# Performance work log

Measured on AMD Instinct MI355X. Metric: run time of the kernel, lower is better.

Reference implementation:

```python
import jax, jax.numpy as jnp
import numpy as np
import math

# static config
NH, HD, HID = 16, 128, 2048
ROT = 64            # head_dim * partial_rotary_factor(0.5)
EPS = 1e-6
GROUPS = 8
CHUNK = 64
THETA = 10000.0
LAYER_IDX, N_LAYERS = 1, 32
B, S = 2, 2048


def _base_slopes(n):
    # power-of-two branch of HF ALiBi slopes
    start = 2 ** (-(2 ** (-(math.log2(n) - 3))))
    return [start * (start ** i) for i in range(n)]

# per-head log-decay (negative): slope = -base * (1 - (l-1)/(L-1) + 1e-5)
SLOPE = jnp.asarray(
    -np.array(_base_slopes(NH), dtype=np.float32)
    * (1.0 - (LAYER_IDX - 1) / (N_LAYERS - 1) + 1e-5),
    dtype=jnp.float32)  # [NH]


def _rmsnorm(x, w):
    return x * jax.lax.rsqrt(jnp.mean(x * x, axis=-1, keepdims=True) + EPS) * w


def _partial_rope(x, positions):
    # x: [B,S,NH,HD]; neox-style rotary on first ROT dims, rest passthrough
    half = ROT // 2
    inv_freq = 1.0 / (THETA ** (jnp.arange(half, dtype=jnp.float32) / half))
    ang = positions.astype(jnp.float32)[:, None] * inv_freq       # [S, half]
    cos = jnp.cos(ang)[None, :, None, :]
    sin = jnp.sin(ang)[None, :, None, :]
    x1, x2, rest = x[..., :half], x[..., half:ROT], x[..., ROT:]
    return jnp.concatenate(
        [x1 * cos - x2 * sin, x2 * cos + x1 * sin, rest], axis=-1)


def setup_inputs() -> dict:
    key = jax.random.key(0)
    ks = jax.random.split(key, 4)
    return {
        'positions': jnp.arange(S, dtype=jnp.int32),
        'hidden_states': jax.random.normal(ks[0], (B, S, HID), jnp.float32),
        'recurrent_state': jnp.zeros((B, NH, HD, HD), jnp.float32),
        'w_qkv': jax.random.normal(ks[1], (HID, 3 * NH * HD), jnp.float32) * 0.02,
        'w_g': jax.random.normal(ks[2], (HID, NH * HD), jnp.float32) * 0.02,
        'w_dense': jax.random.normal(ks[3], (NH * HD, HID), jnp.float32) * 0.02,
        'q_norm_w': jnp.ones((HD,), jnp.float32),
        'k_norm_w': jnp.ones((HD,), jnp.float32),
        'g_norm_w': jnp.ones((NH * HD,), jnp.float32),
    }


def reference(positions, hidden_states, recurrent_state, w_qkv, w_g, w_dense,
              q_norm_w, k_norm_w, g_norm_w):
    # fused QKV projection
    qkv = hidden_states @ w_qkv                       # [B,S,3*NH*HD]
    q, k, v = jnp.split(qkv, 3, axis=-1)
    q = q.reshape(B, S, NH, HD)
    k = k.reshape(B, S, NH, HD)
    v = v.reshape(B, S, NH, HD)

    # QK RMSNorm then partial rotary
    q = _partial_rope(_rmsnorm(q, q_norm_w), positions)
    k = _partial_rope(_rmsnorm(k, k_norm_w), positions)

    # chunked ALiBi-decayed linear attention:
    #   S_t = lam * S_{t-1} + k_t v_t^T ; o_t = q_t S_t, lam = exp(slope)
    NC = S // CHUNK
    qc = q.reshape(B, NC, CHUNK, NH, HD).transpose(1, 0, 3, 2, 4)  # [NC,B,NH,C,HD]
    kc = k.reshape(B, NC, CHUNK, NH, HD).transpose(1, 0, 3, 2, 4)
    vc = v.reshape(B, NC, CHUNK, NH, HD).transpose(1, 0, 3, 2, 4)

    t = jnp.arange(CHUNK, dtype=jnp.float32)
    # intra-chunk causal decay mask lam^(i-j), i>=j: [NH,C,C]
    dec_mask = jnp.where(t[:, None] >= t[None, :],
                         jnp.exp(SLOPE[:, None, None] * (t[:, None] - t[None, :])),
                         0.0)
    q_dec = jnp.exp(SLOPE[:, None] * (t[None, :] + 1.0))            # [NH,C] lam^(i+1)
    k_dec = jnp.exp(SLOPE[:, None] * (CHUNK - 1.0 - t[None, :]))    # [NH,C] lam^(C-1-j)
    lam_C = jnp.exp(SLOPE * CHUNK)                                   # [NH]

    def step(state, inp):
        qb, kb, vb = inp                                  # [B,NH,C,HD]
        scores = jnp.einsum('bhid,bhjd->bhij', qb, kb) * dec_mask[None]
        o_intra = jnp.einsum('bhij,bhjd->bhid', scores, vb)
        o_inter = jnp.einsum('bhid,bhde->bhie', qb * q_dec[None, :, :, None], state)
        new_state = (state * lam_C[None, :, None, None]
                     + jnp.einsum('bhjd,bhje->bhde', kb * k_dec[None, :, :, None], vb))
        return new_state, o_intra + o_inter

    _, o = jax.lax.scan(step, recurrent_state, (qc, kc, vc))  # o: [NC,B,NH,C,HD]
    o = o.transpose(1, 0, 3, 2, 4).reshape(B, S, NH * HD)

    # GroupRMSNorm on attention output, sigmoid gate, output projection
    og = o.reshape(B, S, GROUPS, (NH * HD) // GROUPS)
    og = og * jax.lax.rsqrt(jnp.mean(og * og, axis=-1, keepdims=True) + EPS)
    o = og.reshape(B, S, NH * HD) * g_norm_w
    o = o * jax.nn.sigmoid(hidden_states @ w_g)
    return o @ w_dense
```

## Files before the change

### kernel.cpp

```cpp
#include <hip/hip_runtime.h>
#include <hip/hip_bf16.h>
#include <math.h>

#define NH   16
#define HD   128
#define HID  2048
#define NKV  6144
#define B_   2
#define S_   2048
#define NC   32
#define CHUNK_ 64
#define GROUPS_ 8

typedef __bf16 bf16_t;
typedef bf16_t bf16x8 __attribute__((ext_vector_type(8)));
typedef float  f32x4  __attribute__((ext_vector_type(4)));

__device__ __forceinline__ float b2f(unsigned int u) {
    union { unsigned int u; float f; } c; c.u = (u & 0xffffu) << 16; return c.f;
}
__device__ __forceinline__ unsigned int f2b(float f) {
    union { float f; unsigned int u; } c; c.f = f;
    unsigned int u = c.u;
    return (u + 0x7fffu + ((u >> 16) & 1u)) >> 16;
}

#define GLOAD_LDS16(gp, lp) __builtin_amdgcn_global_load_lds(                     \
    (const __attribute__((address_space(1))) void*)(gp),                          \
    (__attribute__((address_space(3))) void*)(lp), 16, 0, 0)

__global__ __launch_bounds__(256) void cvt_bf16(const float* __restrict__ in,
                                                unsigned short* __restrict__ out, int n8)
{
    int i = blockIdx.x * 256 + threadIdx.x;
    if (i >= n8) return;
    const float4* p = (const float4*)in + (size_t)i * 2;
    float4 a = p[0], b = p[1];
    uint4 o;
    o.x = f2b(a.x) | (f2b(a.y) << 16);
    o.y = f2b(a.z) | (f2b(a.w) << 16);
    o.z = f2b(b.x) | (f2b(b.y) << 16);
    o.w = f2b(b.z) | (f2b(b.w) << 16);
    ((uint4*)out)[i] = o;
}

__global__ __launch_bounds__(256) void transpose_cvt(const float* __restrict__ in,
                                                     unsigned short* __restrict__ out,
                                                     int Kdim, int Ndim)
{
    __shared__ float tile[32][33];
    int ntx = Ndim >> 5;
    int bx = blockIdx.x % ntx;
    int by = blockIdx.x / ntx;
    int lx = threadIdx.x & 31, ly = threadIdx.x >> 5;
    int r0 = by * 32, c0 = bx * 32;
    #pragma unroll
    for (int r = 0; r < 4; ++r)
        tile[ly + r * 8][lx] = in[(size_t)(r0 + ly + r * 8) * Ndim + c0 + lx];
    __syncthreads();
    #pragma unroll
    for (int r = 0; r < 4; ++r)
        out[(size_t)(c0 + ly + r * 8) * Kdim + r0 + lx] = (unsigned short)f2b(tile[lx][ly + r * 8]);
}


__device__ __forceinline__ void ld_fr4(bf16x8 (&d)[4][2], const bf16_t* b, int s0, int ri) {
    #pragma unroll
    for (int i = 0; i < 4; ++i)
        #pragma unroll
        for (int k = 0; k < 2; ++k)
            d[i][k] = *(const bf16x8*)(b + (((s0 + i) * 2 + k) << 9) + ri);
}
__device__ __forceinline__ void ld_fr2(bf16x8 (&d)[2][2], const bf16_t* b, int s0, int ri) {
    #pragma unroll
    for (int i = 0; i < 2; ++i)
        #pragma unroll
        for (int k = 0; k < 2; ++k)
            d[i][k] = *(const bf16x8*)(b + (((s0 + i) * 2 + k) << 9) + ri);
}
__device__ __forceinline__ void mfma_quad(f32x4 (&a)[4][2], const bf16x8 (&af)[4][2],
                                          const bf16x8 (&bv)[2][2]) {
    #pragma unroll
    for (int mt = 0; mt < 4; ++mt)
        #pragma unroll
        for (int nt = 0; nt < 2; ++nt)
            #pragma unroll
            for (int ks = 0; ks < 2; ++ks)
                a[mt][nt] = __builtin_amdgcn_mfma_f32_16x16x32_bf16(af[mt][ks], bv[nt][ks], a[mt][nt], 0, 0, 0);
}

#define BAR()     asm volatile("s_barrier" ::: "memory")
#define VMCNT0()  asm volatile("s_waitcnt vmcnt(0)" ::: "memory")

__global__ __launch_bounds__(512, 2) void gemm_qg_256(const bf16_t* __restrict__ A,
                                                      const bf16_t* __restrict__ Bt,
                                                      unsigned short* __restrict__ Cq,
                                                      unsigned short* __restrict__ Cg)
{
    __shared__ bf16_t Asm[2][2][8192];
    __shared__ bf16_t Bsm[2][2][8192];
    const int K  = HID;
    const int NT = K / 64;

    int tid  = threadIdx.x;
    int wave = tid >> 6, lane = tid & 63;
    int wm = wave >> 2, wn = wave & 3;
    int l16 = lane & 15, quad = lane >> 4;
    int wm4 = wm * 4, wn2 = wn * 2;

    int bid = blockIdx.x;
    int xcd = bid & 7, idx = bid >> 3;
    int by  = (xcd >> 2) * 8 + (idx >> 3);
    int bx  = (xcd & 3) * 8 + (idx & 7);

    int rd_in = ((l16 << 5) | (quad << 3)) ^ (((l16 >> 3) & 1) << 4);

    int ch = lane ^ ((lane & 32) >> 4);
    int rr = ch >> 2;
    int cc = (ch & 3) * 8;

    const bf16_t* aSrc0 = A  + (size_t)(by * 256 +       wave * 16 + rr) * K + cc;
    const bf16_t* aSrc1 = A  + (size_t)(by * 256 + 128 + wave * 16 + rr) * K + cc;
    const bf16_t* bSrc0 = Bt + (size_t)(bx * 256 +       wave * 16 + rr) * K + cc;
    const bf16_t* bSrc1 = Bt + (size_t)(bx * 256 + 128 + wave * 16 + rr) * K + cc;

#define STAGE_A(h, t) do {                                                        \
        const bf16_t* _g = ((h) ? aSrc1 : aSrc0) + (size_t)(t) * 64;              \
        bf16_t* _l = &Asm[(t) & 1][(h)][wave * 1024 + lane * 8];                  \
        GLOAD_LDS16(_g,      _l);                                                 \
        GLOAD_LDS16(_g + 32, _l + 512); } while (0)
#define STAGE_B(h, t) do {                                                        \
        const bf16_t* _g = ((h) ? bSrc1 : bSrc0) + (size_t)(t) * 64;              \
        bf16_t* _l = &Bsm[(t) & 1][(h)][wave * 1024 + lane * 8];                  \
        GLOAD_LDS16(_g,      _l);                                                 \
        GLOAD_LDS16(_g + 32, _l + 512); } while (0)

    f32x4 acc[2][2][4][2];
    #pragma unroll
    for (int a0 = 0; a0 < 2; ++a0)
        #pragma unroll
        for (int a1 = 0; a1 < 2; ++a1)
            #pragma unroll
            for (int a2 = 0; a2 < 4; ++a2)
                #pragma unroll
                for (int a3 = 0; a3 < 2; ++a3) { f32x4 z = {0.f,0.f,0.f,0.f}; acc[a0][a1][a2][a3] = z; }

    STAGE_A(0, 0); STAGE_B(0, 0); STAGE_A(1, 0); STAGE_B(1, 0);
    VMCNT0();
    BAR();

    #pragma unroll 2
    for (int t = 0; t < NT - 1; ++t) {
        const int buf = t & 1;
        STAGE_A(0, t + 1); STAGE_B(0, t + 1); STAGE_A(1, t + 1); STAGE_B(1, t + 1);
        {
            bf16x8 afA[4][2], afB[4][2], bf0[2][2], bf1[2][2];
            ld_fr4(afA, &Asm[buf][0][0], wm4, rd_in);
            ld_fr2(bf0, &Bsm[buf][0][0], wn2, rd_in);
            mfma_quad(acc[0][0], afA, bf0);
            ld_fr2(bf1, &Bsm[buf][1][0], wn2, rd_in);
            mfma_quad(acc[0][1], afA, bf1);
            ld_fr4(afB, &Asm[buf][1][0], wm4, rd_in);
            mfma_quad(acc[1][1], afB, bf1);
            mfma_quad(acc[1][0], afB, bf0);
        }
        VMCNT0();
        BAR();
    }
    {
        const int buf = (NT - 1) & 1;
        bf16x8 afA[4][2], afB[4][2], bf0[2][2], bf1[2][2];
        ld_fr4(afA, &Asm[buf][0][0], wm4, rd_in);
        ld_fr2(bf0, &Bsm[buf][0][0], wn2, rd_in);
        mfma_quad(acc[0][0], afA, bf0);
        ld_fr2(bf1, &Bsm[buf][1][0], wn2, rd_in);
        mfma_quad(acc[0][1], afA, bf1);
        ld_fr4(afB, &Asm[buf][1][0], wm4, rd_in);
        mfma_quad(acc[1][1], afB, bf1);
        mfma_quad(acc[1][0], afB, bf0);
    }
#undef STAGE_A
#undef STAGE_B

    unsigned short* Cc; int Nn, colbase;
    if (bx < 24) { Cc = Cq; Nn = NKV; colbase = bx * 256; }
    else         { Cc = Cg; Nn = HID; colbase = bx * 256 - NKV; }
    int row0 = by * 256 + wm * 64 + quad * 4;
    int col0 = colbase + wn * 32 + l16;
    #pragma unroll
    for (int mh = 0; mh < 2; ++mh)
        #pragma unroll
        for (int nh = 0; nh < 2; ++nh)
            #pragma unroll
            for (int mt = 0; mt < 4; ++mt)
                #pragma unroll
                for (int nt = 0; nt < 2; ++nt) {
                    int col = col0 + nh * 128 + nt * 16;
                    #pragma unroll
                    for (int r = 0; r < 4; ++r) {
                        int row = row0 + mh * 128 + mt * 16 + r;
                        Cc[(size_t)row * Nn + col] = (unsigned short)f2b(acc[mh][nh][mt][nt][r]);
                    }
                }
}

__global__ __launch_bounds__(256, 2) void gemm_out_128(const bf16_t* __restrict__ A,
                                                       const bf16_t* __restrict__ Bt,
                                                       float* __restrict__ C)
{
    __shared__ bf16_t As[2][4096];
    __shared__ bf16_t Bs[2][4096];
    const int K  = HID;
    const int NT = K / 32;

    int tid  = threadIdx.x;
    int wave = tid >> 6, lane = tid & 63;
    int wm2 = wave >> 1, wn2 = wave & 1;
    int l16 = lane & 15, quad = lane >> 4;
    int w2 = wave * 2;

    int bid = blockIdx.x;
    int xcd = bid & 7, idx = bid >> 3;
    int by  = (xcd >> 1) * 8 + (idx >> 3);
    int bx  = (xcd & 1) * 8 + (idx & 7);

    int rd_in = ((l16 << 5) | (quad << 3)) ^ (((l16 >> 3) & 1) << 4);
    int ch = lane ^ ((lane & 32) >> 4);
    int rr = ch >> 2;
    int cc = (ch & 3) * 8;

    const bf16_t* aSrc = A  + (size_t)(by * 128 + w2 * 16 + rr) * K + cc;
    const bf16_t* bSrc = Bt + (size_t)(bx * 128 + w2 * 16 + rr) * K + cc;

#define OSTAGE(t) do {                                                            \
        const int nb_ = (t) & 1;                                                  \
        const bf16_t* _ga = aSrc + (size_t)(t) * 32;                              \
        const bf16_t* _gb = bSrc + (size_t)(t) * 32;                              \
        GLOAD_LDS16(_ga,                  &As[nb_][w2 * 512 + lane * 8]);         \
        GLOAD_LDS16(_ga + (size_t)16 * K, &As[nb_][w2 * 512 + 512 + lane * 8]);   \
        GLOAD_LDS16(_gb,                  &Bs[nb_][w2 * 512 + lane * 8]);         \
        GLOAD_LDS16(_gb + (size_t)16 * K, &Bs[nb_][w2 * 512 + 512 + lane * 8]); } while (0)

    f32x4 acc[4][4];
    #pragma unroll
    for (int i = 0; i < 4; ++i)
        #pragma unroll
        for (int j = 0; j < 4; ++j) { f32x4 z = {0.f,0.f,0.f,0.f}; acc[i][j] = z; }

#define OCOMP(t) do {                                                             \
        const int b_ = (t) & 1;                                                   \
        bf16x8 af_[4], bf_[4];                                                    \
        _Pragma("unroll")                                                         \
        for (int i = 0; i < 4; ++i)                                               \
            af_[i] = *(const bf16x8*)(&As[b_][((wm2 * 4 + i) << 9) + rd_in]);     \
        _Pragma("unroll")                                                         \
        for (int j = 0; j < 4; ++j)                                               \
            bf_[j] = *(const bf16x8*)(&Bs[b_][((wn2 * 4 + j) << 9) + rd_in]);     \
        _Pragma("unroll")                                                         \
        for (int i = 0; i < 4; ++i)                                               \
            _Pragma("unroll")                                                     \
            for (int j = 0; j < 4; ++j)                                           \
                acc[i][j] = __builtin_amdgcn_mfma_f32_16x16x32_bf16(af_[i], bf_[j], acc[i][j], 0, 0, 0); } while (0)

    OSTAGE(0);
    VMCNT0();
    BAR();
    #pragma unroll 2
    for (int t = 0; t < NT - 1; ++t) {
        OSTAGE(t + 1);
        OCOMP(t);
        VMCNT0();
        BAR();
    }
    OCOMP(NT - 1);
#undef OSTAGE
#undef OCOMP

    #pragma unroll
    for (int i = 0; i < 4; ++i)
        #pragma unroll
        for (int j = 0; j < 4; ++j) {
            int col = bx * 128 + wn2 * 64 + j * 16 + l16;
            #pragma unroll
            for (int r = 0; r < 4; ++r) {
                int row = by * 128 + wm2 * 64 + i * 16 + quad * 4 + r;
                C[(size_t)row * HID + col] = acc[i][j][r];
            }
        }
}

__global__ __launch_bounds__(256) void norm_rope(unsigned short* __restrict__ qkv,
                                                 const int* __restrict__ positions,
                                                 const float* __restrict__ qw,
                                                 const float* __restrict__ kw)
{
    int bs = blockIdx.x;
    int s  = bs & (S_ - 1);
    int tid = threadIdx.x;
    int l16 = tid & 15;
    unsigned short* base = qkv + (size_t)bs * NKV;
    float pos = (float)positions[s];

    #pragma unroll
    for (int p = 0; p < 2; ++p) {
        int rr = p * 16 + (tid >> 4);
        int qk = rr >> 4;
        int h  = rr & 15;
        unsigned short* row = base + qk * HID + h * HD;
        const float* w = qk ? kw : qw;
        uint4 v = *(const uint4*)(row + l16 * 8);
        float x[8];
        x[0] = b2f(v.x); x[1] = b2f(v.x >> 16);
        x[2] = b2f(v.y); x[3] = b2f(v.y >> 16);
        x[4] = b2f(v.z); x[5] = b2f(v.z >> 16);
        x[6] = b2f(v.w); x[7] = b2f(v.w >> 16);
        float ss = 0.f;
        #pragma unroll
        for (int t = 0; t < 8; ++t) ss += x[t] * x[t];
        ss += __shfl_xor(ss, 1); ss += __shfl_xor(ss, 2);
        ss += __shfl_xor(ss, 4); ss += __shfl_xor(ss, 8);
        float inv = rsqrtf(ss * (1.0f / 128.0f) + 1e-6f);
        float n[8];
        #pragma unroll
        for (int t = 0; t < 8; ++t) n[t] = x[t] * inv * w[l16 * 8 + t];
        float pr[8];
        #pragma unroll
        for (int t = 0; t < 8; ++t) pr[t] = __shfl_xor(n[t], 4);
        if (l16 < 8) {
            #pragma unroll
            for (int t = 0; t < 8; ++t) {
                int dim = l16 * 8 + t;
                int i = dim & 31;
                float ang = pos * exp2f(-(float)i * 0.4152410118609203f);
                float cs = cosf(ang), sn = sinf(ang);
                n[t] = (dim < 32) ? (n[t] * cs - pr[t] * sn) : (n[t] * cs + pr[t] * sn);
            }
        }
        uint4 o;
        o.x = f2b(n[0]) | (f2b(n[1]) << 16);
        o.y = f2b(n[2]) | (f2b(n[3]) << 16);
        o.z = f2b(n[4]) | (f2b(n[5]) << 16);
        o.w = f2b(n[6]) | (f2b(n[7]) << 16);
        *(uint4*)(row + l16 * 8) = o;
    }
}

__global__ __launch_bounds__(256) void chunk_kv(const unsigned short* __restrict__ qkv,
                                                unsigned short* __restrict__ wbuf)
{
    __shared__ unsigned short kt[128 * 72];
    __shared__ unsigned short vt[128 * 72];
    int bi = blockIdx.x;
    int c = bi & 31, bh = bi >> 5, h = bh & 15, b = bh >> 4;
    int tid = threadIdx.x;
    float slope = -exp2f(-0.5f * (float)(h + 1)) * (1.0f + 1e-5f);

    const unsigned short* kbase = qkv + ((size_t)(b * S_ + c * CHUNK_)) * NKV + HID + h * HD;
    const unsigned short* vbase = kbase + HID;

    for (int idx = tid; idx < 4096; idx += 256) {
        int j = idx >> 6, p = idx & 63;
        unsigned int ku = *(const unsigned int*)(kbase + (size_t)j * NKV + p * 2);
        kt[(2 * p) * 72 + j]     = (unsigned short)(ku & 0xffffu);
        kt[(2 * p + 1) * 72 + j] = (unsigned short)(ku >> 16);
        float kd = expf(slope * (float)(63 - j));
        unsigned int vu = *(const unsigned int*)(vbase + (size_t)j * NKV + p * 2);
        vt[(2 * p) * 72 + j]     = (unsigned short)f2b(b2f(vu) * kd);
        vt[(2 * p + 1) * 72 + j] = (unsigned short)f2b(b2f(vu >> 16) * kd);
    }
    __syncthreads();

    int lane = tid & 63, wave = tid >> 6;
    int wm = (wave >> 1) * 64;
    int wn = (wave & 1) * 64;
    int l16 = lane & 15, quad = lane >> 4;

    f32x4 acc[4][4];
    #pragma unroll
    for (int i = 0; i < 4; ++i)
        #pragma unroll
        for (int j = 0; j < 4; ++j) { f32x4 z = {0.f,0.f,0.f,0.f}; acc[i][j] = z; }

    #pragma unroll
    for (int ks = 0; ks < 64; ks += 32) {
        bf16x8 af[4], bf[4];
        #pragma unroll
        for (int t = 0; t < 4; ++t) {
            af[t] = *(const bf16x8*)((const bf16_t*)vt + (wm + t * 16 + l16) * 72 + ks + quad * 8);
            bf[t] = *(const bf16x8*)((const bf16_t*)kt + (wn + t * 16 + l16) * 72 + ks + quad * 8);
        }
        #pragma unroll
        for (int mt = 0; mt < 4; ++mt)
            #pragma unroll
            for (int nt = 0; nt < 4; ++nt)
                acc[mt][nt] = __builtin_amdgcn_mfma_f32_16x16x32_bf16(af[mt], bf[nt], acc[mt][nt], 0, 0, 0);
    }

    unsigned short* wp = wbuf + ((size_t)bi << 14);
    #pragma unroll
    for (int mt = 0; mt < 4; ++mt)
        #pragma unroll
        for (int nt = 0; nt < 4; ++nt) {
            int dcol = wn + nt * 16 + l16;
            #pragma unroll
            for (int r = 0; r < 4; ++r) {
                int erow = wm + mt * 16 + quad * 4 + r;
                wp[(size_t)erow * 128 + dcol] = (unsigned short)f2b(acc[mt][nt][r]);
            }
        }
}

__global__ __launch_bounds__(256) void state_scan(const unsigned short* __restrict__ wbuf,
                                                  const float* __restrict__ rs0,
                                                  unsigned short* __restrict__ stbuf)
{
    int bi = blockIdx.x;
    int es = bi & 15, bh = bi >> 4, h = bh & 15, b = bh >> 4;
    int tid = threadIdx.x;
    float slope = -exp2f(-0.5f * (float)(h + 1)) * (1.0f + 1e-5f);
    float lam = expf(slope * 64.0f);

    int e  = es * 8 + (tid >> 5);
    int d0 = (tid & 31) * 4;

    float S[4];
    const float* rp = rs0 + ((size_t)(b * NH + h)) * HD * HD + e;
    #pragma unroll
    for (int t = 0; t < 4; ++t) S[t] = rp[(size_t)(d0 + t) * HD];

    size_t off = (size_t)e * 128 + d0;
    size_t base = (((size_t)bh * NC) << 14) + off;
    uint2 w0 = *(const uint2*)(wbuf + base);
    uint2 w1 = *(const uint2*)(wbuf + base + (1 << 14));
    for (int c = 0; c < NC; ++c) {
        uint2 o;
        o.x = f2b(S[0]) | (f2b(S[1]) << 16);
        o.y = f2b(S[2]) | (f2b(S[3]) << 16);
        *(uint2*)(stbuf + base) = o;
        uint2 w2 = w1;
        if (c + 2 < NC) w2 = *(const uint2*)(wbuf + base + (2 << 14));
        S[0] = S[0] * lam + b2f(w0.x);
        S[1] = S[1] * lam + b2f(w0.x >> 16);
        S[2] = S[2] * lam + b2f(w0.y);
        S[3] = S[3] * lam + b2f(w0.y >> 16);
        w0 = w1; w1 = w2;
        base += (1 << 14);
    }
}

__global__ __launch_bounds__(256) void chunk_out(const unsigned short* __restrict__ qkv,
                                                 const unsigned short* __restrict__ stbuf,
                                                 unsigned short* __restrict__ obuf)
{
    __shared__ unsigned short qs[64 * 136];
    __shared__ unsigned short kss[64 * 136];
    __shared__ unsigned short vt[128 * 72];
    __shared__ unsigned short sc[64 * 72];

    int bi = blockIdx.x;
    int c = bi & 31, bh = bi >> 5, h = bh & 15, b = bh >> 4;
    int tid = threadIdx.x;
    float slope = -exp2f(-0.5f * (float)(h + 1)) * (1.0f + 1e-5f);

    int lane = tid & 63, wave = tid >> 6;
    int l16 = lane & 15, quad = lane >> 4;
    int wn3 = wave * 32;

    const unsigned short* stp = stbuf + (((size_t)bh * NC + c) << 14);
    bf16x8 bsf[4][2];
    #pragma unroll
    for (int ksp4 = 0; ksp4 < 4; ++ksp4)
        #pragma unroll
        for (int nt = 0; nt < 2; ++nt)
            bsf[ksp4][nt] = *(const bf16x8*)((const bf16_t*)stp +
                (size_t)(wn3 + nt * 16 + l16) * 128 + ksp4 * 32 + quad * 8);

    const unsigned short* qrow = qkv + ((size_t)(b * S_ + c * CHUNK_)) * NKV + h * HD;
    const unsigned short* krow = qrow + HID;
    for (int idx = tid; idx < 1024; idx += 256) {
        int row = idx >> 4, c8 = (idx & 15) * 8;
        *(uint4*)(qs  + row * 136 + c8) = *(const uint4*)(qrow + (size_t)row * NKV + c8);
        *(uint4*)(kss + row * 136 + c8) = *(const uint4*)(krow + (size_t)row * NKV + c8);
    }
    const unsigned short* vbase = qrow + 2 * HID;
    for (int idx = tid; idx < 4096; idx += 256) {
        int j = idx >> 6, p = idx & 63;
        unsigned int vu = *(const unsigned int*)(vbase + (size_t)j * NKV + p * 2);
        vt[(2 * p) * 72 + j]     = (unsigned short)(vu & 0xffffu);
        vt[(2 * p + 1) * 72 + j] = (unsigned short)(vu >> 16);
    }
    __syncthreads();

    {
        f32x4 accS[4];
        #pragma unroll
        for (int t = 0; t < 4; ++t) { f32x4 z = {0.f,0.f,0.f,0.f}; accS[t] = z; }
        #pragma unroll
        for (int ksp = 0; ksp < 128; ksp += 32) {
            bf16x8 aq = *(const bf16x8*)((const bf16_t*)qs + (wave * 16 + l16) * 136 + ksp + quad * 8);
            #pragma unroll
            for (int nt = 0; nt < 4; ++nt) {
                bf16x8 bk = *(const bf16x8*)((const bf16_t*)kss + (nt * 16 + l16) * 136 + ksp + quad * 8);
                accS[nt] = __builtin_amdgcn_mfma_f32_16x16x32_bf16(aq, bk, accS[nt], 0, 0, 0);
            }
        }
        float ad[4];
        #pragma unroll
        for (int r = 0; r < 4; ++r) ad[r] = expf(slope * (float)(wave * 16 + quad * 4 + r));
        #pragma unroll
        for (int nt = 0; nt < 4; ++nt) {
            int j = nt * 16 + l16;
            float bd = expf(-slope * (float)j);
            #pragma unroll
            for (int r = 0; r < 4; ++r) {
                int i = wave * 16 + quad * 4 + r;
                float v = (i >= j) ? accS[nt][r] * ad[r] * bd : 0.0f;
                sc[i * 72 + j] = (unsigned short)f2b(v);
            }
        }
    }
    __syncthreads();

    f32x4 accI[4][2], accE[4][2];
    #pragma unroll
    for (int i = 0; i < 4; ++i)
        #pragma unroll
        for (int j = 0; j < 2; ++j) { f32x4 z = {0.f,0.f,0.f,0.f}; accI[i][j] = z; accE[i][j] = z; }

    #pragma unroll
    for (int ksp = 0; ksp < 64; ksp += 32) {
        bf16x8 as[4], bv[2];
        #pragma unroll
        for (int mt = 0; mt < 4; ++mt)
            as[mt] = *(const bf16x8*)((const bf16_t*)sc + (mt * 16 + l16) * 72 + ksp + quad * 8);
        #pragma unroll
        for (int nt = 0; nt < 2; ++nt)
            bv[nt] = *(const bf16x8*)((const bf16_t*)vt + (wn3 + nt * 16 + l16) * 72 + ksp + quad * 8);
        #pragma unroll
        for (int mt = 0; mt < 4; ++mt)
            #pragma unroll
            for (int nt = 0; nt < 2; ++nt)
                accI[mt][nt] = __builtin_amdgcn_mfma_f32_16x16x32_bf16(as[mt], bv[nt], accI[mt][nt], 0, 0, 0);
    }
    #pragma unroll
    for (int ksp4 = 0; ksp4 < 4; ++ksp4) {
        bf16x8 aq[4];
        #pragma unroll
        for (int mt = 0; mt < 4; ++mt)
            aq[mt] = *(const bf16x8*)((const bf16_t*)qs + (mt * 16 + l16) * 136 + ksp4 * 32 + quad * 8);
        #pragma unroll
        for (int mt = 0; mt < 4; ++mt)
            #pragma unroll
            for (int nt = 0; nt < 2; ++nt)
                accE[mt][nt] = __builtin_amdgcn_mfma_f32_16x16x32_bf16(aq[mt], bsf[ksp4][nt], accE[mt][nt], 0, 0, 0);
    }

    #pragma unroll
    for (int mt = 0; mt < 4; ++mt) {
        #pragma unroll
        for (int r = 0; r < 4; ++r) {
            int i = mt * 16 + quad * 4 + r;
            float qd = expf(slope * (float)(i + 1));
            int orow = b * S_ + c * CHUNK_ + i;
            #pragma unroll
            for (int nt = 0; nt < 2; ++nt) {
                int col = h * HD + wn3 + nt * 16 + l16;
                float o = accI[mt][nt][r] + qd * accE[mt][nt][r];
                obuf[(size_t)orow * 2048 + col] = (unsigned short)f2b(o);
            }
        }
    }
}

__global__ __launch_bounds__(256) void gnorm_gate(const unsigned short* __restrict__ o,
                                                  unsigned short* __restrict__ gate,
                                                  const float* __restrict__ gw)
{
    int row = blockIdx.x >> 3;
    int g   = blockIdx.x & 7;
    int col = g * 256 + threadIdx.x;
    size_t idx = (size_t)row * 2048 + col;
    float ov = b2f(o[idx]);
    float ss = ov * ov;
    #pragma unroll
    for (int off = 32; off > 0; off >>= 1) ss += __shfl_xor(ss, off);
    __shared__ float part[4];
    if ((threadIdx.x & 63) == 0) part[threadIdx.x >> 6] = ss;
    __syncthreads();
    float tot = part[0] + part[1] + part[2] + part[3];
    float inv = rsqrtf(tot * (1.0f / 256.0f) + 1e-6f);
    float gv = b2f(gate[idx]);
    float sig = 1.0f / (1.0f + expf(-gv));
    gate[idx] = (unsigned short)f2b(ov * inv * gw[col] * sig);
}

extern "C" void kernel_launch(void* const* d_in, const int* in_sizes, int n_in,
                              void* d_out, int out_size, void* d_ws, size_t ws_size,
                              hipStream_t stream) {
    const int*   positions = (const int*)d_in[0];
    const float* hidden    = (const float*)d_in[1];
    const float* rstate    = (const float*)d_in[2];
    const float* w_qkv     = (const float*)d_in[3];
    const float* w_g       = (const float*)d_in[4];
    const float* w_dense   = (const float*)d_in[5];
    const float* q_norm_w  = (const float*)d_in[6];
    const float* k_norm_w  = (const float*)d_in[7];
    const float* g_norm_w  = (const float*)d_in[8];
    float* out = (float*)d_out;

    const int MR = B_ * S_;

    char* w = (char*)d_ws;
    unsigned short* qkv  = (unsigned short*)w;            w += (size_t)MR * NKV * 2;
    unsigned short* gbuf = (unsigned short*)w;            w += (size_t)MR * 2048 * 2;
    unsigned short* wdT  = (unsigned short*)w;            w += (size_t)HID * HID * 2;
    char* regionA = w;                                    w += (size_t)MR * HID * 2 + (size_t)8192 * HID * 2;
    char* regionB = w;
    unsigned short* hbf   = (unsigned short*)regionA;
    unsigned short* btQG  = (unsigned short*)(regionA + (size_t)MR * HID * 2);
    unsigned short* wqT   = btQG;
    unsigned short* wgT   = btQG + (size_t)NKV * HID;
    unsigned short* stbuf = (unsigned short*)regionA;
    unsigned short* wbuf  = (unsigned short*)regionB;
    unsigned short* obuf  = (unsigned short*)regionB;

    cvt_bf16<<<dim3((MR * HID / 8 + 255) / 256), dim3(256), 0, stream>>>(hidden, hbf, MR * HID / 8);
    transpose_cvt<<<dim3((HID / 32) * (NKV / 32)), dim3(256), 0, stream>>>(w_qkv, wqT, HID, NKV);
    transpose_cvt<<<dim3((HID / 32) * (HID / 32)), dim3(256), 0, stream>>>(w_g, wgT, HID, HID);
    transpose_cvt<<<dim3((HID / 32) * (HID / 32)), dim3(256), 0, stream>>>(w_dense, wdT, HID, HID);

    gemm_qg_256<<<dim3(512), dim3(512), 0, stream>>>(
        (const bf16_t*)hbf, (const bf16_t*)btQG, qkv, gbuf);
    norm_rope<<<dim3(B_ * S_), dim3(256), 0, stream>>>(qkv, positions, q_norm_w, k_norm_w);

    chunk_kv<<<dim3(B_ * NH * NC), dim3(256), 0, stream>>>(qkv, wbuf);
    state_scan<<<dim3(B_ * NH * 16), dim3(256), 0, stream>>>(wbuf, rstate, stbuf);
    chunk_out<<<dim3(B_ * NH * NC), dim3(256), 0, stream>>>(qkv, stbuf, obuf);

    gnorm_gate<<<dim3(MR * GROUPS_), dim3(256), 0, stream>>>(obuf, gbuf, g_norm_w);
    gemm_out_128<<<dim3(512), dim3(256), 0, stream>>>(
        (const bf16_t*)gbuf, (const bf16_t*)wdT, out);
}
```

Before: 424.1 us.

## Fuse norm/rope into chunk kernels, merge weight transposes, vectorize gate norm

Removes the standalone norm_rope kernel. Q/K RMSNorm and partial RoPE are now applied in shared memory inside chunk_kv and chunk_out, so qkv is no longer read and rewritten in a separate pass. The two QKV/G weight transposes are merged into one launch. The state buffer layout becomes MFMA-fragment-friendly so state_scan can use 16-byte loads with deeper prefetch and chunk_out can read state fragments contiguously. gnorm_gate is rewritten to process a full row per block with 8-wide vectors. The cost is that K normalization is recomputed in both chunk kernels, and the chunk kernels use more shared memory.

```diff
diff --git a/kernel.cpp b/kernel.cpp
--- a/kernel.cpp
+++ b/kernel.cpp
@@ -28,6 +28,9 @@
 #define GLOAD_LDS16(gp, lp) __builtin_amdgcn_global_load_lds(                     \
     (const __attribute__((address_space(1))) void*)(gp),                          \
     (__attribute__((address_space(3))) void*)(lp), 16, 0, 0)
+
+#define BAR()     asm volatile("s_barrier" ::: "memory")
+#define VMCNT0()  asm volatile("s_waitcnt vmcnt(0)" ::: "memory")
 
 __global__ __launch_bounds__(256) void cvt_bf16(const float* __restrict__ in,
                                                 unsigned short* __restrict__ out, int n8)
@@ -63,6 +66,26 @@
         out[(size_t)(c0 + ly + r * 8) * Kdim + r0 + lx] = (unsigned short)f2b(tile[lx][ly + r * 8]);
 }
 
+__global__ __launch_bounds__(256) void transpose_qg(const float* __restrict__ wq,
+                                                    const float* __restrict__ wg,
+                                                    unsigned short* __restrict__ out)
+{
+    __shared__ float tile[32][33];
+    int bx = blockIdx.x & 255;
+    int by = blockIdx.x >> 8;
+    int lx = threadIdx.x & 31, ly = threadIdx.x >> 5;
+    const float* in; int Ndim, c0;
+    if (bx < 192) { in = wq; Ndim = NKV; c0 = bx * 32; }
+    else          { in = wg; Ndim = HID; c0 = (bx - 192) * 32; }
+    int r0 = by * 32;
+    #pragma unroll
+    for (int r = 0; r < 4; ++r)
+        tile[ly + r * 8][lx] = in[(size_t)(r0 + ly + r * 8) * Ndim + c0 + lx];
+    __syncthreads();
+    #pragma unroll
+    for (int r = 0; r < 4; ++r)
+        out[(size_t)(bx * 32 + ly + r * 8) * HID + r0 + lx] = (unsigned short)f2b(tile[lx][ly + r * 8]);
+}
 
 __device__ __forceinline__ void ld_fr4(bf16x8 (&d)[4][2], const bf16_t* b, int s0, int ri) {
     #pragma unroll
@@ -88,9 +111,6 @@
             for (int ks = 0; ks < 2; ++ks)
                 a[mt][nt] = __builtin_amdgcn_mfma_f32_16x16x32_bf16(af[mt][ks], bv[nt][ks], a[mt][nt], 0, 0, 0);
 }
-
-#define BAR()     asm volatile("s_barrier" ::: "memory")
-#define VMCNT0()  asm volatile("s_waitcnt vmcnt(0)" ::: "memory")
 
 __global__ __launch_bounds__(512, 2) void gemm_qg_256(const bf16_t* __restrict__ A,
                                                       const bf16_t* __restrict__ Bt,
@@ -114,7 +134,6 @@
     int bx  = (xcd & 3) * 8 + (idx & 7);
 
     int rd_in = ((l16 << 5) | (quad << 3)) ^ (((l16 >> 3) & 1) << 4);
-
     int ch = lane ^ ((lane & 32) >> 4);
     int rr = ch >> 2;
     int cc = (ch & 3) * 8;
@@ -289,65 +308,51 @@
         }
 }
 
-__global__ __launch_bounds__(256) void norm_rope(unsigned short* __restrict__ qkv,
-                                                 const int* __restrict__ positions,
-                                                 const float* __restrict__ qw,
-                                                 const float* __restrict__ kw)
-{
-    int bs = blockIdx.x;
-    int s  = bs & (S_ - 1);
-    int tid = threadIdx.x;
-    int l16 = tid & 15;
-    unsigned short* base = qkv + (size_t)bs * NKV;
-    float pos = (float)positions[s];
-
-    #pragma unroll
-    for (int p = 0; p < 2; ++p) {
-        int rr = p * 16 + (tid >> 4);
-        int qk = rr >> 4;
-        int h  = rr & 15;
-        unsigned short* row = base + qk * HID + h * HD;
-        const float* w = qk ? kw : qw;
-        uint4 v = *(const uint4*)(row + l16 * 8);
-        float x[8];
-        x[0] = b2f(v.x); x[1] = b2f(v.x >> 16);
-        x[2] = b2f(v.y); x[3] = b2f(v.y >> 16);
-        x[4] = b2f(v.z); x[5] = b2f(v.z >> 16);
-        x[6] = b2f(v.w); x[7] = b2f(v.w >> 16);
-        float ss = 0.f;
-        #pragma unroll
-        for (int t = 0; t < 8; ++t) ss += x[t] * x[t];
-        ss += __shfl_xor(ss, 1); ss += __shfl_xor(ss, 2);
-        ss += __shfl_xor(ss, 4); ss += __shfl_xor(ss, 8);
-        float inv = rsqrtf(ss * (1.0f / 128.0f) + 1e-6f);
-        float n[8];
-        #pragma unroll
-        for (int t = 0; t < 8; ++t) n[t] = x[t] * inv * w[l16 * 8 + t];
-        float pr[8];
-        #pragma unroll
-        for (int t = 0; t < 8; ++t) pr[t] = __shfl_xor(n[t], 4);
-        if (l16 < 8) {
-            #pragma unroll
-            for (int t = 0; t < 8; ++t) {
-                int dim = l16 * 8 + t;
-                int i = dim & 31;
-                float ang = pos * exp2f(-(float)i * 0.4152410118609203f);
-                float cs = cosf(ang), sn = sinf(ang);
-                n[t] = (dim < 32) ? (n[t] * cs - pr[t] * sn) : (n[t] * cs + pr[t] * sn);
-            }
-        }
-        uint4 o;
-        o.x = f2b(n[0]) | (f2b(n[1]) << 16);
-        o.y = f2b(n[2]) | (f2b(n[3]) << 16);
-        o.z = f2b(n[4]) | (f2b(n[5]) << 16);
-        o.w = f2b(n[6]) | (f2b(n[7]) << 16);
-        *(uint4*)(row + l16 * 8) = o;
-    }
+__device__ __forceinline__ void nr_row(unsigned short* rowp, const float* __restrict__ w,
+                                       float pos, int ln)
+{
+    uint4 v = *(const uint4*)(rowp + ln * 8);
+    float x[8];
+    x[0] = b2f(v.x); x[1] = b2f(v.x >> 16);
+    x[2] = b2f(v.y); x[3] = b2f(v.y >> 16);
+    x[4] = b2f(v.z); x[5] = b2f(v.z >> 16);
+    x[6] = b2f(v.w); x[7] = b2f(v.w >> 16);
+    float ss = 0.f;
+    #pragma unroll
+    for (int t = 0; t < 8; ++t) ss += x[t] * x[t];
+    ss += __shfl_xor(ss, 1); ss += __shfl_xor(ss, 2);
+    ss += __shfl_xor(ss, 4); ss += __shfl_xor(ss, 8);
+    float inv = rsqrtf(ss * (1.0f / 128.0f) + 1e-6f);
+    float n[8];
+    #pragma unroll
+    for (int t = 0; t < 8; ++t) n[t] = x[t] * inv * w[ln * 8 + t];
+    float pr[8];
+    #pragma unroll
+    for (int t = 0; t < 8; ++t) pr[t] = __shfl_xor(n[t], 4);
+    if (ln < 8) {
+        #pragma unroll
+        for (int t = 0; t < 8; ++t) {
+            int dim = ln * 8 + t;
+            int i = dim & 31;
+            float ang = pos * exp2f(-(float)i * 0.4152410118609203f);
+            float cs = cosf(ang), sn = sinf(ang);
+            n[t] = (dim < 32) ? (n[t] * cs - pr[t] * sn) : (n[t] * cs + pr[t] * sn);
+        }
+    }
+    uint4 o;
+    o.x = f2b(n[0]) | (f2b(n[1]) << 16);
+    o.y = f2b(n[2]) | (f2b(n[3]) << 16);
+    o.z = f2b(n[4]) | (f2b(n[5]) << 16);
+    o.w = f2b(n[6]) | (f2b(n[7]) << 16);
+    *(uint4*)(rowp + ln * 8) = o;
 }
 
 __global__ __launch_bounds__(256) void chunk_kv(const unsigned short* __restrict__ qkv,
+                                                const int* __restrict__ positions,
+                                                const float* __restrict__ kw,
                                                 unsigned short* __restrict__ wbuf)
 {
+    __shared__ unsigned short kraw[64 * 136];
     __shared__ unsigned short kt[128 * 72];
     __shared__ unsigned short vt[128 * 72];
     int bi = blockIdx.x;
@@ -358,11 +363,12 @@
     const unsigned short* kbase = qkv + ((size_t)(b * S_ + c * CHUNK_)) * NKV + HID + h * HD;
     const unsigned short* vbase = kbase + HID;
 
+    for (int idx = tid; idx < 1024; idx += 256) {
+        int row = idx >> 4, c8 = (idx & 15) * 8;
+        *(uint4*)(kraw + row * 136 + c8) = *(const uint4*)(kbase + (size_t)row * NKV + c8);
+    }
     for (int idx = tid; idx < 4096; idx += 256) {
         int j = idx >> 6, p = idx & 63;
-        unsigned int ku = *(const unsigned int*)(kbase + (size_t)j * NKV + p * 2);
-        kt[(2 * p) * 72 + j]     = (unsigned short)(ku & 0xffffu);
-        kt[(2 * p + 1) * 72 + j] = (unsigned short)(ku >> 16);
         float kd = expf(slope * (float)(63 - j));
         unsigned int vu = *(const unsigned int*)(vbase + (size_t)j * NKV + p * 2);
         vt[(2 * p) * 72 + j]     = (unsigned short)f2b(b2f(vu) * kd);
@@ -370,6 +376,25 @@
     }
     __syncthreads();
 
+    {
+        int rp = tid >> 4, ln = tid & 15;
+        #pragma unroll
+        for (int pass = 0; pass < 4; ++pass) {
+            int row = pass * 16 + rp;
+            float pos = (float)positions[c * CHUNK_ + row];
+            nr_row(kraw + row * 136, kw, pos, ln);
+        }
+    }
+    __syncthreads();
+
+    for (int idx = tid; idx < 4096; idx += 256) {
+        int j = idx >> 6, p = idx & 63;
+        unsigned int ku = *(const unsigned int*)(kraw + j * 136 + p * 2);
+        kt[(2 * p) * 72 + j]     = (unsigned short)(ku & 0xffffu);
+        kt[(2 * p + 1) * 72 + j] = (unsigned short)(ku >> 16);
+    }
+    __syncthreads();
+
     int lane = tid & 63, wave = tid >> 6;
     int wm = (wave >> 1) * 64;
     int wn = (wave & 1) * 64;
@@ -401,11 +426,12 @@
     for (int mt = 0; mt < 4; ++mt)
         #pragma unroll
         for (int nt = 0; nt < 4; ++nt) {
-            int dcol = wn + nt * 16 + l16;
+            int cid = ((wave >> 1) * 4 + mt) * 4 + (wave & 1) * 2 + (nt >> 1);
+            int pos = ((nt & 1) * 2 + (l16 >> 3)) * 128 + (l16 & 7);
             #pragma unroll
             for (int r = 0; r < 4; ++r) {
-                int erow = wm + mt * 16 + quad * 4 + r;
-                wp[(size_t)erow * 128 + dcol] = (unsigned short)f2b(acc[mt][nt][r]);
+                int e15 = quad * 4 + r;
+                wp[cid * 512 + pos + e15 * 8] = (unsigned short)f2b(acc[mt][nt][r]);
             }
         }
 }
@@ -415,40 +441,51 @@
                                                   unsigned short* __restrict__ stbuf)
 {
     int bi = blockIdx.x;
-    int es = bi & 15, bh = bi >> 4, h = bh & 15, b = bh >> 4;
+    int s = bi & 7, bh = bi >> 3, h = bh & 15, b = bh >> 4;
     int tid = threadIdx.x;
     float slope = -exp2f(-0.5f * (float)(h + 1)) * (1.0f + 1e-5f);
     float lam = expf(slope * 64.0f);
 
-    int e  = es * 8 + (tid >> 5);
-    int d0 = (tid & 31) * 4;
-
-    float S[4];
+    int T  = s * 256 + tid;
+    int cid = T >> 6, lc = T & 63;
+    int e  = (cid >> 2) * 16 + (lc & 15);
+    int d0 = (cid & 3) * 32 + (lc >> 4) * 8;
+
+    float S[8];
     const float* rp = rs0 + ((size_t)(b * NH + h)) * HD * HD + e;
     #pragma unroll
-    for (int t = 0; t < 4; ++t) S[t] = rp[(size_t)(d0 + t) * HD];
-
-    size_t off = (size_t)e * 128 + d0;
-    size_t base = (((size_t)bh * NC) << 14) + off;
-    uint2 w0 = *(const uint2*)(wbuf + base);
-    uint2 w1 = *(const uint2*)(wbuf + base + (1 << 14));
-    for (int c = 0; c < NC; ++c) {
-        uint2 o;
-        o.x = f2b(S[0]) | (f2b(S[1]) << 16);
-        o.y = f2b(S[2]) | (f2b(S[3]) << 16);
-        *(uint2*)(stbuf + base) = o;
-        uint2 w2 = w1;
-        if (c + 2 < NC) w2 = *(const uint2*)(wbuf + base + (2 << 14));
-        S[0] = S[0] * lam + b2f(w0.x);
-        S[1] = S[1] * lam + b2f(w0.x >> 16);
-        S[2] = S[2] * lam + b2f(w0.y);
-        S[3] = S[3] * lam + b2f(w0.y >> 16);
-        w0 = w1; w1 = w2;
-        base += (1 << 14);
+    for (int t = 0; t < 8; ++t) S[t] = rp[(size_t)(d0 + t) * HD];
+
+    size_t base = (((size_t)bh * NC) << 14) + (size_t)T * 8;
+    uint4 wr[4];
+    #pragma unroll
+    for (int i = 0; i < 4; ++i)
+        wr[i] = *(const uint4*)(wbuf + base + ((size_t)i << 14));
+    for (int c0 = 0; c0 < NC; c0 += 4) {
+        #pragma unroll
+        for (int u = 0; u < 4; ++u) {
+            uint4 o;
+            o.x = f2b(S[0]) | (f2b(S[1]) << 16);
+            o.y = f2b(S[2]) | (f2b(S[3]) << 16);
+            o.z = f2b(S[4]) | (f2b(S[5]) << 16);
+            o.w = f2b(S[6]) | (f2b(S[7]) << 16);
+            *(uint4*)(stbuf + base) = o;
+            uint4 wc = wr[u];
+            if (c0 + 4 + u < NC)
+                wr[u] = *(const uint4*)(wbuf + base + ((size_t)4 << 14));
+            S[0] = S[0] * lam + b2f(wc.x); S[1] = S[1] * lam + b2f(wc.x >> 16);
+            S[2] = S[2] * lam + b2f(wc.y); S[3] = S[3] * lam + b2f(wc.y >> 16);
+            S[4] = S[4] * lam + b2f(wc.z); S[5] = S[5] * lam + b2f(wc.z >> 16);
+            S[6] = S[6] * lam + b2f(wc.w); S[7] = S[7] * lam + b2f(wc.w >> 16);
+            base += (size_t)1 << 14;
+        }
     }
 }
 
 __global__ __launch_bounds__(256) void chunk_out(const unsigned short* __restrict__ qkv,
+                                                 const int* __restrict__ positions,
+                                                 const float* __restrict__ qw,
+                                                 const float* __restrict__ kw,
                                                  const unsigned short* __restrict__ stbuf,
                                                  unsigned short* __restrict__ obuf)
 {
@@ -473,7 +510,7 @@
         #pragma unroll
         for (int nt = 0; nt < 2; ++nt)
             bsf[ksp4][nt] = *(const bf16x8*)((const bf16_t*)stp +
-                (size_t)(wn3 + nt * 16 + l16) * 128 + ksp4 * 32 + quad * 8);
+                (((wave * 2 + nt) * 4 + ksp4) << 9) + lane * 8);
 
     const unsigned short* qrow = qkv + ((size_t)(b * S_ + c * CHUNK_)) * NKV + h * HD;
     const unsigned short* krow = qrow + HID;
@@ -492,6 +529,18 @@
     __syncthreads();
 
     {
+        int rp = tid >> 4, ln = tid & 15;
+        #pragma unroll
+        for (int pass = 0; pass < 4; ++pass) {
+            int row = pass * 16 + rp;
+            float pos = (float)positions[c * CHUNK_ + row];
+            nr_row(qs  + row * 136, qw, pos, ln);
+            nr_row(kss + row * 136, kw, pos, ln);
+        }
+    }
+    __syncthreads();
+
+    {
         f32x4 accS[4];
         #pragma unroll
         for (int t = 0; t < 4; ++t) { f32x4 z = {0.f,0.f,0.f,0.f}; accS[t] = z; }
@@ -576,22 +625,42 @@
                                                   unsigned short* __restrict__ gate,
                                                   const float* __restrict__ gw)
 {
-    int row = blockIdx.x >> 3;
-    int g   = blockIdx.x & 7;
-    int col = g * 256 + threadIdx.x;
-    size_t idx = (size_t)row * 2048 + col;
-    float ov = b2f(o[idx]);
-    float ss = ov * ov;
-    #pragma unroll
-    for (int off = 32; off > 0; off >>= 1) ss += __shfl_xor(ss, off);
-    __shared__ float part[4];
-    if ((threadIdx.x & 63) == 0) part[threadIdx.x >> 6] = ss;
-    __syncthreads();
-    float tot = part[0] + part[1] + part[2] + part[3];
-    float inv = rsqrtf(tot * (1.0f / 256.0f) + 1e-6f);
-    float gv = b2f(gate[idx]);
-    float sig = 1.0f / (1.0f + expf(-gv));
-    gate[idx] = (unsigned short)f2b(ov * inv * gw[col] * sig);
+    int row = blockIdx.x;
+    int tid = threadIdx.x;
+    size_t base8 = (size_t)row * 256 + tid;
+    uint4 ov = ((const uint4*)o)[base8];
+    uint4 gv = ((const uint4*)gate)[base8];
+    float x[8];
+    x[0] = b2f(ov.x); x[1] = b2f(ov.x >> 16);
+    x[2] = b2f(ov.y); x[3] = b2f(ov.y >> 16);
+    x[4] = b2f(ov.z); x[5] = b2f(ov.z >> 16);
+    x[6] = b2f(ov.w); x[7] = b2f(ov.w >> 16);
+    float ss = 0.f;
+    #pragma unroll
+    for (int t = 0; t < 8; ++t) ss += x[t] * x[t];
+    ss += __shfl_xor(ss, 1); ss += __shfl_xor(ss, 2); ss += __shfl_xor(ss, 4);
+    ss += __shfl_xor(ss, 8); ss += __shfl_xor(ss, 16);
+    float inv = rsqrtf(ss * (1.0f / 256.0f) + 1e-6f);
+    const float4* gwp = (const float4*)(gw + tid * 8);
+    float4 w0 = gwp[0], w1 = gwp[1];
+    float g[8];
+    g[0] = b2f(gv.x); g[1] = b2f(gv.x >> 16);
+    g[2] = b2f(gv.y); g[3] = b2f(gv.y >> 16);
+    g[4] = b2f(gv.z); g[5] = b2f(gv.z >> 16);
+    g[6] = b2f(gv.w); g[7] = b2f(gv.w >> 16);
+    float wv[8] = {w0.x, w0.y, w0.z, w0.w, w1.x, w1.y, w1.z, w1.w};
+    float r[8];
+    #pragma unroll
+    for (int t = 0; t < 8; ++t) {
+        float sig = 1.0f / (1.0f + expf(-g[t]));
+        r[t] = x[t] * inv * wv[t] * sig;
+    }
+    uint4 out;
+    out.x = f2b(r[0]) | (f2b(r[1]) << 16);
+    out.y = f2b(r[2]) | (f2b(r[3]) << 16);
+    out.z = f2b(r[4]) | (f2b(r[5]) << 16);
+    out.w = f2b(r[6]) | (f2b(r[7]) << 16);
+    ((uint4*)gate)[base8] = out;
 }
 
 extern "C" void kernel_launch(void* const* d_in, const int* in_sizes, int n_in,
@@ -618,26 +687,22 @@
     char* regionB = w;
     unsigned short* hbf   = (unsigned short*)regionA;
     unsigned short* btQG  = (unsigned short*)(regionA + (size_t)MR * HID * 2);
-    unsigned short* wqT   = btQG;
-    unsigned short* wgT   = btQG + (size_t)NKV * HID;
     unsigned short* stbuf = (unsigned short*)regionA;
     unsigned short* wbuf  = (unsigned short*)regionB;
     unsigned short* obuf  = (unsigned short*)regionB;
 
     cvt_bf16<<<dim3((MR * HID / 8 + 255) / 256), dim3(256), 0, stream>>>(hidden, hbf, MR * HID / 8);
-    transpose_cvt<<<dim3((HID / 32) * (NKV / 32)), dim3(256), 0, stream>>>(w_qkv, wqT, HID, NKV);
-    transpose_cvt<<<dim3((HID / 32) * (HID / 32)), dim3(256), 0, stream>>>(w_g, wgT, HID, HID);
+    transpose_qg<<<dim3(64 * 256), dim3(256), 0, stream>>>(w_qkv, w_g, btQG);
     transpose_cvt<<<dim3((HID / 32) * (HID / 32)), dim3(256), 0, stream>>>(w_dense, wdT, HID, HID);
 
     gemm_qg_256<<<dim3(512), dim3(512), 0, stream>>>(
         (const bf16_t*)hbf, (const bf16_t*)btQG, qkv, gbuf);
-    norm_rope<<<dim3(B_ * S_), dim3(256), 0, stream>>>(qkv, positions, q_norm_w, k_norm_w);
-
-    chunk_kv<<<dim3(B_ * NH * NC), dim3(256), 0, stream>>>(qkv, wbuf);
-    state_scan<<<dim3(B_ * NH * 16), dim3(256), 0, stream>>>(wbuf, rstate, stbuf);
-    chunk_out<<<dim3(B_ * NH * NC), dim3(256), 0, stream>>>(qkv, stbuf, obuf);
-
-    gnorm_gate<<<dim3(MR * GROUPS_), dim3(256), 0, stream>>>(obuf, gbuf, g_norm_w);
+
+    chunk_kv<<<dim3(B_ * NH * NC), dim3(256), 0, stream>>>(qkv, positions, k_norm_w, wbuf);
+    state_scan<<<dim3(B_ * NH * 8), dim3(256), 0, stream>>>(wbuf, rstate, stbuf);
+    chunk_out<<<dim3(B_ * NH * NC), dim3(256), 0, stream>>>(qkv, positions, q_norm_w, k_norm_w, stbuf, obuf);
+
+    gnorm_gate<<<dim3(MR), dim3(256), 0, stream>>>(obuf, gbuf, g_norm_w);
     gemm_out_128<<<dim3(512), dim3(256), 0, stream>>>(
         (const bf16_t*)gbuf, (const bf16_t*)wdT, out);
 }
```

After: 473.4 us. 11.6% more time.
